# Optimization experiments

Measured on AMD Instinct MI355X. Metric: run time of the kernel, lower is better.

## Reference

```python
import jax, jax.numpy as jnp
import numpy as np
from jax import lax


def _conv1x1(x, w, b=None):
    # x: [N,C,H,W], w: [O,C]
    y = jnp.einsum('nchw,oc->nohw', x, w)
    if b is not None:
        y = y + b[None, :, None, None]
    return y


def _bn(x, g, b, rm, rv):
    # eval-mode BatchNorm2d, eps=1e-5 (torch default)
    inv = g / jnp.sqrt(rv + 1e-5)
    return x * inv[None, :, None, None] + (b - rm * inv)[None, :, None, None]


def setup_inputs() -> dict:
    key = jax.random.key(0)
    ks = jax.random.split(key, 32)
    N, C1, C2, H, W = 16, 256, 256, 64, 64
    mid = C2 // 16  # local_att reduction=16
    f32 = jnp.float32
    def nrm(k, shp, s=0.05):
        return s * jax.random.normal(k, shp, f32)
    return dict(
        x1=jax.random.normal(ks[0], (N, C1, H, W), f32),
        x2=jax.random.normal(ks[1], (N, C2, H, W), f32),
        conv1_w=nrm(ks[2], (C2, C1)), conv1_b=nrm(ks[3], (C2,)),
        conv2_w=nrm(ks[4], (C2, C2)), conv2_b=nrm(ks[5], (C2,)),
        conv3_w=nrm(ks[6], (C2, C2)), conv3_b=nrm(ks[7], (C2,)),
        conv4_w=nrm(ks[8], (C2, C2)), conv4_b=nrm(ks[9], (C2,)),
        conv4g_w=nrm(ks[10], (1, C2)), conv4g_b=nrm(ks[11], (1,)),
        bn_g=1.0 + nrm(ks[12], (C2,)), bn_b=nrm(ks[13], (C2,)),
        bn_rm=nrm(ks[14], (C2,)), bn_rv=1.0 + 0.1 * jax.random.uniform(ks[15], (C2,), f32),
        gamma=jax.random.normal(ks[16], (C2, 1, 1), f32), beta=jnp.zeros((C2, 1, 1), f32),
        gate_w=nrm(ks[17], (C2, C2)), gate_b=nrm(ks[18], (C2,)),
        dw_w=nrm(ks[19], (C2, 1, 3, 3)), dw_b=nrm(ks[20], (C2,)),
        interact_w=nrm(ks[21], (C2 // 4, C2 // 4)), interact_b=0.5 + nrm(ks[22], (C2 // 4,)),
        ca_w=nrm(ks[23], (1, 1, 5)),  # channel_att conv1d kernel, k=5 for C=256
        la1_w=nrm(ks[24], (mid, C2)),
        la_bn_g=1.0 + nrm(ks[25], (mid,)), la_bn_b=nrm(ks[26], (mid,)),
        la_bn_rm=nrm(ks[27], (mid,)), la_bn_rv=1.0 + 0.1 * jax.random.uniform(ks[28], (mid,), f32),
        fh_w=nrm(ks[29], (C2, mid)), fw_w=nrm(ks[30], (C2, mid)),
    )


def reference(x1, x2, conv1_w, conv1_b, conv2_w, conv2_b, conv3_w, conv3_b,
              conv4_w, conv4_b, conv4g_w, conv4g_b, bn_g, bn_b, bn_rm, bn_rv,
              gamma, beta, gate_w, gate_b, dw_w, dw_b, interact_w, interact_b,
              ca_w, la1_w, la_bn_g, la_bn_b, la_bn_rm, la_bn_rv, fh_w, fw_w):
    N, _, H, W = x1.shape
    C = conv1_w.shape[0]
    g1 = _conv1x1(x1, conv1_w, conv1_b)
    w1 = jax.nn.sigmoid(_bn(g1, bn_g, bn_b, bn_rm, bn_rv))
    g2 = _conv1x1(x2, conv2_w, conv2_b)
    w2 = jax.nn.sigmoid(_bn(g2, bn_g, bn_b, bn_rm, bn_rv))
    XG = g1 + g2

    # channel_att: GAP -> conv1d(k=5) across channels -> sigmoid gate
    y = XG.mean((2, 3))[:, None, :]  # [N,1,C]
    y = lax.conv_general_dilated(y, ca_w, (1,), [(2, 2)],
                                 dimension_numbers=('NCH', 'OIH', 'NCH'))
    temp = XG * jax.nn.sigmoid(y[:, 0, :])[:, :, None, None]

    # spatial sigmoid gate then 4-way group interact + softmax reweight
    Xs = jax.nn.sigmoid(_conv1x1(XG, conv4g_w, conv4g_b)) * XG
    C4 = C // 4
    Xr = Xs.reshape(N, 4, C4, H, W)
    o1 = jnp.einsum('ngchw,oc->ngohw', Xr, interact_w) + interact_b[None, None, :, None, None]
    xmap = o1.reshape(N, 4, 1, C4 * H * W)
    xav = xmap / xmap.mean(-1, keepdims=True)
    soft = jax.nn.softmax(xav, axis=2)  # softmax over size-1 dim -> ones (faithful)
    out = (soft.reshape(N, 4, C4, H, W) * Xr).reshape(N, C, H, W)

    # per-group (16) normalization using X_GOBAL stats (std unbiased, ddof=1)
    GN = 16
    xs = XG.reshape(N, GN, -1)
    mu = xs.mean(-1, keepdims=True)
    sd = jnp.std(xs, axis=-1, keepdims=True, ddof=1)
    x_gui = ((out.reshape(N, GN, -1) - mu) / (sd + 1e-10)).reshape(N, C, H, W)
    x_gui = x_gui * gamma[None] + beta[None]

    # threshold masks vs global-avg sigmoid reweights
    rw = jax.nn.sigmoid(XG.mean((2, 3), keepdims=True))  # [N,C,1,1]
    up1 = rw >= w1
    up2 = rw >= w2
    zero = jnp.zeros((), XG.dtype)
    x_up = jnp.where(up1, XG, zero) + jnp.where(up2, XG, zero)
    x_low = jnp.where(~up1, XG, zero) + jnp.where(~up2, XG, zero)

    # low branch: dwconv3x3 -> 1x1 -> channel-softmax gate
    dw = lax.conv_general_dilated(x_low, dw_w, (1, 1), [(1, 1), (1, 1)],
                                  dimension_numbers=('NCHW', 'OIHW', 'NCHW'),
                                  feature_group_count=C) + dw_b[None, :, None, None]
    x11 = _conv1x1(dw, conv3_w, conv3_b)
    gate = jax.nn.softmax(jax.nn.relu(x_low.mean((2, 3)) @ gate_w.T + gate_b), axis=1)
    xL = x11 * gate[:, :, None, None] + _conv1x1(x_up, conv4_w, conv4_b) + x_gui + temp

    # local_att (coordinate attention)
    xh = jnp.swapaxes(xL.mean(3, keepdims=True), 2, 3)  # [N,C,1,H]
    xw = xL.mean(2, keepdims=True)                       # [N,C,1,W]
    yc = jax.nn.relu(_bn(_conv1x1(jnp.concatenate([xh, xw], 3), la1_w),
                         la_bn_g, la_bn_b, la_bn_rm, la_bn_rv))
    sh = jax.nn.sigmoid(_conv1x1(jnp.swapaxes(yc[..., :H], 2, 3), fh_w))  # [N,C,H,1]
    sw = jax.nn.sigmoid(_conv1x1(yc[..., H:], fw_w))                      # [N,C,1,W]
    return xL * sh * sw
```

## Files before the change

kernel.cpp:

```cpp
#include <hip/hip_runtime.h>
#include <cstddef>
#include <cstdint>

constexpr int NN = 16, CC = 256, HH = 64, WW = 64, HW = 64 * 64;
constexpr size_t FSZ = (size_t)NN * CC * HW;

typedef short bf16x8 __attribute__((ext_vector_type(8)));
typedef float f32x4 __attribute__((ext_vector_type(4)));

__device__ __forceinline__ float sigmoidf_(float x) { return 1.f / (1.f + expf(-x)); }

__device__ __forceinline__ unsigned short bf16_rne(float f) {
    uint32_t u = __builtin_bit_cast(uint32_t, f);
    u += 0x7FFFu + ((u >> 16) & 1u);
    return (unsigned short)(u >> 16);
}
__device__ __forceinline__ float bf16_tof(unsigned short h) {
    uint32_t u = ((uint32_t)h) << 16;
    return __builtin_bit_cast(float, u);
}


__global__ __launch_bounds__(256) void wsplit_kernel(
    const float* __restrict__ w1, const float* __restrict__ w2,
    const float* __restrict__ w3, const float* __restrict__ w4,
    unsigned short* __restrict__ w1h, unsigned short* __restrict__ w1m, unsigned short* __restrict__ w1l,
    unsigned short* __restrict__ w2h, unsigned short* __restrict__ w2m, unsigned short* __restrict__ w2l,
    unsigned short* __restrict__ w4h, unsigned short* __restrict__ w4l,
    unsigned short* __restrict__ w3b,
    float* __restrict__ zstat, float* __restrict__ zspix) {
    const int i = blockIdx.x * 256 + threadIdx.x;
    const int o = i >> 8, c = i & 255;
    const size_t fo = ((size_t)((o >> 4) * 8 + (c >> 5))) * 512 +
                      (size_t)(((c & 31) >> 3) * 128 + (o & 15) * 8 + (c & 7));
    {
        float x = w1[i];
        unsigned short h = bf16_rne(x); float r = x - bf16_tof(h);
        unsigned short m = bf16_rne(r); float r2 = r - bf16_tof(m);
        w1h[fo] = h; w1m[fo] = m; w1l[fo] = bf16_rne(r2);
    }
    {
        float x = w2[i];
        unsigned short h = bf16_rne(x); float r = x - bf16_tof(h);
        unsigned short m = bf16_rne(r); float r2 = r - bf16_tof(m);
        w2h[fo] = h; w2m[fo] = m; w2l[fo] = bf16_rne(r2);
    }
    {
        float x = w4[i];
        unsigned short h = bf16_rne(x); float r = x - bf16_tof(h);
        w4h[fo] = h; w4l[fo] = bf16_rne(r);
    }
    w3b[fo] = bf16_rne(w3[i]);
    if (i < 8192) zstat[i] = 0.f;
    zspix[i] = 0.f;
}

template <int NS>
__global__ __launch_bounds__(256) void tsplit_kernel(const float* __restrict__ X,
                                                     unsigned short* __restrict__ O0,
                                                     unsigned short* __restrict__ O1,
                                                     unsigned short* __restrict__ O2) {
    const int hw0 = blockIdx.x * 64, c0 = blockIdx.y * 64, n = blockIdx.z;
    __shared__ float sT[64][65];
    const int tid = threadIdx.x;
    {
        const int hwl = (tid & 15) << 2;
        const int cl = tid >> 4;
#pragma unroll
        for (int p = 0; p < 4; ++p) {
            const int c = cl + p * 16;
            const float4 v = *(const float4*)(X + ((size_t)(n * CC + c0 + c)) * HW + hw0 + hwl);
            sT[c][hwl] = v.x; sT[c][hwl + 1] = v.y; sT[c][hwl + 2] = v.z; sT[c][hwl + 3] = v.w;
        }
    }
    __syncthreads();
    const int hwl = tid >> 2, cb = (tid & 3) << 4;
    unsigned short h[16], m[16], l[16];
#pragma unroll
    for (int j = 0; j < 16; ++j) {
        const float x = sT[cb + j][hwl];
        const unsigned short hh = bf16_rne(x);
        h[j] = hh;
        if (NS >= 2) {
            const float r = x - bf16_tof(hh);
            const unsigned short mm = bf16_rne(r);
            m[j] = mm;
            if (NS >= 3) l[j] = bf16_rne(r - bf16_tof(mm));
        }
    }
    const size_t ob = ((size_t)(n * HW + hw0 + hwl)) * 256 + c0 + cb;
    *(int4*)(O0 + ob) = *(int4*)&h[0]; *(int4*)(O0 + ob + 8) = *(int4*)&h[8];
    if (NS >= 2) { *(int4*)(O1 + ob) = *(int4*)&m[0]; *(int4*)(O1 + ob + 8) = *(int4*)&m[8]; }
    if (NS >= 3) { *(int4*)(O2 + ob) = *(int4*)&l[0]; *(int4*)(O2 + ob + 8) = *(int4*)&l[8]; }
}

template <int NS>
__device__ __forceinline__ void mfma_core5(const unsigned short* __restrict__ X0,
                                           const unsigned short* __restrict__ X1,
                                           const unsigned short* __restrict__ X2,
                                           const unsigned short* __restrict__ W0,
                                           const unsigned short* __restrict__ W1,
                                           const unsigned short* __restrict__ W2,
                                           int n, int hw0, int o0, f32x4 (&acc)[2][4]) {
    __shared__ unsigned short sX[2][NS][64][40];
    const int tid = threadIdx.x;
    const int lane = tid & 63, wv = tid >> 6, quad = lane >> 4, nlo = lane & 15;
    const int srow = tid >> 2, skoff = (tid & 3) << 3;
    const unsigned short* Xs[3] = {X0, X1, X2};
    const unsigned short* Ws[3] = {W0, W1, W2};
    const size_t xg = ((size_t)(n * HW + hw0 + srow)) * 256 + skoff;
    const unsigned short* wp[NS];
#pragma unroll
    for (int s = 0; s < NS; ++s)
        wp[s] = Ws[s] + ((size_t)((o0 >> 4) + wv) * 8) * 512 + (size_t)lane * 8;

    bf16x8 af[2][NS][2];
#pragma unroll
    for (int s = 0; s < NS; ++s)
        *(int4*)&sX[0][s][srow][skoff] = *(const int4*)(Xs[s] + xg);
#pragma unroll
    for (int s = 0; s < NS; ++s)
#pragma unroll
        for (int f = 0; f < 2; ++f)
            af[0][s][f] = *(const bf16x8*)(wp[s] + ((size_t)(f * 32)) * 512);
    __syncthreads();

#pragma unroll
    for (int ks = 0; ks < 8; ++ks) {
        const int cur = ks & 1;
        int4 nx[NS];
        if (ks < 7) {
#pragma unroll
            for (int s = 0; s < NS; ++s) nx[s] = *(const int4*)(Xs[s] + xg + (ks + 1) * 32);
#pragma unroll
            for (int s = 0; s < NS; ++s)
#pragma unroll
                for (int f = 0; f < 2; ++f)
                    af[cur ^ 1][s][f] = *(const bf16x8*)(wp[s] + ((size_t)(f * 32 + ks + 1)) * 512);
        }
#pragma unroll
        for (int nt = 0; nt < 4; ++nt) {
            bf16x8 bfr[NS];
#pragma unroll
            for (int s = 0; s < NS; ++s) bfr[s] = *(const bf16x8*)&sX[cur][s][nt * 16 + nlo][quad * 8];
#pragma unroll
            for (int f = 0; f < 2; ++f) {
                if (NS == 3) {
                    acc[f][nt] = __builtin_amdgcn_mfma_f32_16x16x32_bf16(af[cur][1][f], bfr[1], acc[f][nt], 0, 0, 0);
                    acc[f][nt] = __builtin_amdgcn_mfma_f32_16x16x32_bf16(af[cur][0][f], bfr[2], acc[f][nt], 0, 0, 0);
                    acc[f][nt] = __builtin_amdgcn_mfma_f32_16x16x32_bf16(af[cur][2][f], bfr[0], acc[f][nt], 0, 0, 0);
                    acc[f][nt] = __builtin_amdgcn_mfma_f32_16x16x32_bf16(af[cur][0][f], bfr[1], acc[f][nt], 0, 0, 0);
                    acc[f][nt] = __builtin_amdgcn_mfma_f32_16x16x32_bf16(af[cur][1][f], bfr[0], acc[f][nt], 0, 0, 0);
                    acc[f][nt] = __builtin_amdgcn_mfma_f32_16x16x32_bf16(af[cur][0][f], bfr[0], acc[f][nt], 0, 0, 0);
                } else if (NS == 2) {
                    acc[f][nt] = __builtin_amdgcn_mfma_f32_16x16x32_bf16(af[cur][0][f], bfr[1], acc[f][nt], 0, 0, 0);
                    acc[f][nt] = __builtin_amdgcn_mfma_f32_16x16x32_bf16(af[cur][1][f], bfr[0], acc[f][nt], 0, 0, 0);
                    acc[f][nt] = __builtin_amdgcn_mfma_f32_16x16x32_bf16(af[cur][0][f], bfr[0], acc[f][nt], 0, 0, 0);
                } else {
                    acc[f][nt] = __builtin_amdgcn_mfma_f32_16x16x32_bf16(af[cur][0][f], bfr[0], acc[f][nt], 0, 0, 0);
                }
            }
        }
        if (ks < 7) {
#pragma unroll
            for (int s = 0; s < NS; ++s) *(int4*)&sX[cur ^ 1][s][srow][skoff] = nx[s];
        }
        __syncthreads();
    }
}

__device__ __forceinline__ void mfma_core_pair(const unsigned short* __restrict__ XUH,
                                               const unsigned short* __restrict__ XUL,
                                               const unsigned short* __restrict__ XDW,
                                               const unsigned short* __restrict__ W4H,
                                               const unsigned short* __restrict__ W4L,
                                               const unsigned short* __restrict__ W3B,
                                               int n, int hw0, int o0,
                                               f32x4 (&acc_a)[2][4], f32x4 (&acc_b)[2][4]) {
    __shared__ unsigned short sX[2][3][64][40];
    const int tid = threadIdx.x;
    const int lane = tid & 63, wv = tid >> 6, quad = lane >> 4, nlo = lane & 15;
    const int srow = tid >> 2, skoff = (tid & 3) << 3;
    const unsigned short* Xs[3] = {XUH, XUL, XDW};
    const unsigned short* Ws[3] = {W4H, W4L, W3B};
    const size_t xg = ((size_t)(n * HW + hw0 + srow)) * 256 + skoff;
    const unsigned short* wp[3];
#pragma unroll
    for (int s = 0; s < 3; ++s)
        wp[s] = Ws[s] + ((size_t)((o0 >> 4) + wv) * 8) * 512 + (size_t)lane * 8;

    bf16x8 af[2][3][2];
#pragma unroll
    for (int s = 0; s < 3; ++s)
        *(int4*)&sX[0][s][srow][skoff] = *(const int4*)(Xs[s] + xg);
#pragma unroll
    for (int s = 0; s < 3; ++s)
#pragma unroll
        for (int f = 0; f < 2; ++f)
            af[0][s][f] = *(const bf16x8*)(wp[s] + ((size_t)(f * 32)) * 512);
    __syncthreads();

#pragma unroll
    for (int ks = 0; ks < 8; ++ks) {
        const int cur = ks & 1;
        int4 nx[3];
        if (ks < 7) {
#pragma unroll
            for (int s = 0; s < 3; ++s) nx[s] = *(const int4*)(Xs[s] + xg + (ks + 1) * 32);
#pragma unroll
            for (int s = 0; s < 3; ++s)
#pragma unroll
                for (int f = 0; f < 2; ++f)
                    af[cur ^ 1][s][f] = *(const bf16x8*)(wp[s] + ((size_t)(f * 32 + ks + 1)) * 512);
        }
#pragma unroll
        for (int nt = 0; nt < 4; ++nt) {
            bf16x8 bfr[3];
#pragma unroll
            for (int s = 0; s < 3; ++s) bfr[s] = *(const bf16x8*)&sX[cur][s][nt * 16 + nlo][quad * 8];
#pragma unroll
            for (int f = 0; f < 2; ++f) {
                acc_a[f][nt] = __builtin_amdgcn_mfma_f32_16x16x32_bf16(af[cur][0][f], bfr[1], acc_a[f][nt], 0, 0, 0);
                acc_a[f][nt] = __builtin_amdgcn_mfma_f32_16x16x32_bf16(af[cur][1][f], bfr[0], acc_a[f][nt], 0, 0, 0);
                acc_a[f][nt] = __builtin_amdgcn_mfma_f32_16x16x32_bf16(af[cur][0][f], bfr[0], acc_a[f][nt], 0, 0, 0);
                acc_b[f][nt] = __builtin_amdgcn_mfma_f32_16x16x32_bf16(af[cur][2][f], bfr[2], acc_b[f][nt], 0, 0, 0);
            }
        }
        if (ks < 7) {
#pragma unroll
            for (int s = 0; s < 3; ++s) *(int4*)&sX[cur ^ 1][s][srow][skoff] = nx[s];
        }
        __syncthreads();
    }
}

template <int NS>
__global__ __launch_bounds__(256, 3) void gemm_mfma_kernel(
    const unsigned short* __restrict__ X0, const unsigned short* __restrict__ X1,
    const unsigned short* __restrict__ X2, const unsigned short* __restrict__ W0,
    const unsigned short* __restrict__ W1, const unsigned short* __restrict__ W2,
    const float* __restrict__ bias, float* __restrict__ Y) {
    const int hw0 = blockIdx.x * 64, o0 = blockIdx.y * 128, n = blockIdx.z;
    f32x4 acc[2][4] = {};
    mfma_core5<NS>(X0, X1, X2, W0, W1, W2, n, hw0, o0, acc);
    const int lane = threadIdx.x & 63, wv = threadIdx.x >> 6;
    const int quad = lane >> 4, nlo = lane & 15;
#pragma unroll
    for (int f = 0; f < 2; ++f) {
        const int om = o0 + f * 64 + wv * 16 + quad * 4;
#pragma unroll
        for (int nt = 0; nt < 4; ++nt) {
            const int hw = hw0 + nt * 16 + nlo;
#pragma unroll
            for (int r = 0; r < 4; ++r) {
                const int o = om + r;
                Y[((size_t)(n * CC + o)) * HW + hw] = acc[f][nt][r] + bias[o];
            }
        }
    }
}

__global__ __launch_bounds__(256, 3) void gemm_xg_kernel(
    const unsigned short* __restrict__ X0, const unsigned short* __restrict__ X1,
    const unsigned short* __restrict__ X2, const unsigned short* __restrict__ W0,
    const unsigned short* __restrict__ W1, const unsigned short* __restrict__ W2,
    const float* __restrict__ bias, const float* __restrict__ g1,
    const float* __restrict__ cgw,
    float* __restrict__ XG, float* __restrict__ sum_c, float* __restrict__ sq_c,
    float* __restrict__ s_pix) {
    const int hw0 = blockIdx.x * 64, o0 = blockIdx.y * 128, n = blockIdx.z;
    f32x4 acc[2][4] = {};
    mfma_core5<3>(X0, X1, X2, W0, W1, W2, n, hw0, o0, acc);
    __shared__ float sRed[4][64];
    const int lane = threadIdx.x & 63, wv = threadIdx.x >> 6;
    const int quad = lane >> 4, nlo = lane & 15;
    float pnt[4] = {0.f, 0.f, 0.f, 0.f};
#pragma unroll
    for (int f = 0; f < 2; ++f) {
        const int om = o0 + f * 64 + wv * 16 + quad * 4;
#pragma unroll
        for (int r = 0; r < 4; ++r) {
            const int o = om + r;
            const float b = bias[o];
            const float wg = cgw[o];
            float s = 0.f, q = 0.f;
#pragma unroll
            for (int nt = 0; nt < 4; ++nt) {
                const int hw = hw0 + nt * 16 + nlo;
                const size_t rowi = ((size_t)(n * CC + o)) * HW + hw;
                const float xgv = acc[f][nt][r] + b + g1[rowi];
                XG[rowi] = xgv;
                s += xgv; q += xgv * xgv;
                pnt[nt] += wg * xgv;
            }
#pragma unroll
            for (int off = 1; off < 16; off <<= 1) { s += __shfl_xor(s, off); q += __shfl_xor(q, off); }
            if (nlo == 0) { atomicAdd(&sum_c[n * CC + o], s); atomicAdd(&sq_c[n * CC + o], q); }
        }
    }
#pragma unroll
    for (int nt = 0; nt < 4; ++nt) {
        float p = pnt[nt];
        p += __shfl_xor(p, 16); p += __shfl_xor(p, 32);
        if (quad == 0) sRed[wv][nt * 16 + nlo] = p;
    }
    __syncthreads();
    if (threadIdx.x < 64) {
        const float s2 = sRed[0][threadIdx.x] + sRed[1][threadIdx.x] +
                         sRed[2][threadIdx.x] + sRed[3][threadIdx.x];
        atomicAdd(&s_pix[n * HW + hw0 + threadIdx.x], s2);
    }
}

__global__ __launch_bounds__(256, 3) void gemm_final_kernel(
    const unsigned short* __restrict__ XUH, const unsigned short* __restrict__ XUL,
    const unsigned short* __restrict__ XDW,
    const unsigned short* __restrict__ W4H, const unsigned short* __restrict__ W4L,
    const unsigned short* __restrict__ W3B,
    const float* __restrict__ b3, const float* __restrict__ b4,
    const float* __restrict__ XG, const float* __restrict__ s_pix,
    const float* __restrict__ cgb,
    const float* __restrict__ gate, const float* __restrict__ ca_sig,
    const float* __restrict__ mu_g, const float* __restrict__ isd_g,
    const float* __restrict__ gamma, const float* __restrict__ beta,
    float* __restrict__ out) {
    const int hw0 = blockIdx.x * 64, o0 = blockIdx.y * 128, n = blockIdx.z;
    f32x4 acc_a[2][4] = {};
    f32x4 acc_b[2][4] = {};
    mfma_core_pair(XUH, XUL, XDW, W4H, W4L, W3B, n, hw0, o0, acc_a, acc_b);
    const int lane = threadIdx.x & 63, wv = threadIdx.x >> 6;
    const int quad = lane >> 4, nlo = lane & 15;
    const float cgb0 = cgb[0];
#pragma unroll
    for (int f = 0; f < 2; ++f) {
        const int om = o0 + f * 64 + wv * 16 + quad * 4;
#pragma unroll
        for (int nt = 0; nt < 4; ++nt) {
            const int hw = hw0 + nt * 16 + nlo;
            const int pix = n * HW + hw;
            const float sp = sigmoidf_(s_pix[pix] + cgb0);
#pragma unroll
            for (int r = 0; r < 4; ++r) {
                const int o = om + r;
                const float g = gate[n * CC + o];
                const float cs = ca_sig[n * CC + o];
                const float mu = mu_g[n * 16 + (o >> 4)];
                const float isd = isd_g[n * 16 + (o >> 4)];
                const size_t rowi = ((size_t)(n * CC + o)) * HW + hw;
                const float xg = XG[rowi];
                const float gui = (sp * xg - mu) * isd * gamma[o] + beta[o];
                out[rowi] = (acc_b[f][nt][r] + b3[o]) * g + (acc_a[f][nt][r] + b4[o]) + gui + xg * cs;
            }
        }
    }
}

__global__ __launch_bounds__(256) void stats2_kernel(const float* __restrict__ sum_c,
                                                     const float* __restrict__ sq_c,
                                                     const float* __restrict__ caw,
                                                     float* __restrict__ rw,
                                                     float* __restrict__ ca_sig,
                                                     float* __restrict__ mu_g,
                                                     float* __restrict__ isd_g,
                                                     float* __restrict__ xlow_sum) {
    const int n = blockIdx.x, c = threadIdx.x;
    __shared__ float m[256];
    const float mean = sum_c[n * CC + c] * (1.f / (float)HW);
    m[c] = mean;
    rw[n * CC + c] = sigmoidf_(mean);
    xlow_sum[n * CC + c] = 0.f;
    __syncthreads();
    float y = 0.f;
#pragma unroll
    for (int k = 0; k < 5; ++k) {
        const int cc = c - 2 + k;
        if (cc >= 0 && cc < 256) y += m[cc] * caw[k];
    }
    ca_sig[n * CC + c] = sigmoidf_(y);
    if (c < 16) {
        float S = 0.f, Q = 0.f;
        for (int j = 0; j < 16; ++j) {
            S += sum_c[n * CC + c * 16 + j];
            Q += sq_c[n * CC + c * 16 + j];
        }
        const float cnt = 65536.f;
        const float mu = S / cnt;
        float var = (Q - S * S / cnt) * (1.f / (cnt - 1.f));
        var = fmaxf(var, 0.f);
        mu_g[n * 16 + c] = mu;
        isd_g[n * 16 + c] = 1.f / (sqrtf(var) + 1e-10f);
    }
}

__global__ __launch_bounds__(256) void masks_split_kernel(
    float* g1_xlow,
    const float* __restrict__ XG,
    const float* __restrict__ rw,
    const float* __restrict__ bng, const float* __restrict__ bnb,
    const float* __restrict__ bnrm, const float* __restrict__ bnrv,
    unsigned short* __restrict__ O0, unsigned short* __restrict__ O1,
    float* __restrict__ xlow_sum) {
    const int hw0 = blockIdx.x * 64, c0 = blockIdx.y * 64, n = blockIdx.z;
    __shared__ float sT[64][65];
    const int tid = threadIdx.x;
    const int cl = tid >> 2;
    const int q = tid & 3;
    const int c = c0 + cl;
    const float inv = bng[c] / sqrtf(bnrv[c] + 1e-5f);
    const float off = bnb[c] - bnrm[c] * inv;
    const float rwv = rw[n * CC + c];
    const size_t rowb = ((size_t)(n * CC + c)) * HW + hw0;
    float lsum = 0.f;
#pragma unroll
    for (int j = 0; j < 4; ++j) {
        const int hwl = q * 4 + j * 16;
        const float4 a = *(const float4*)(g1_xlow + rowb + hwl);
        const float4 x = *(const float4*)(XG + rowb + hwl);
        const float* ap = &a.x; const float* xp = &x.x;
        float4 xlv;
        float* xlp = &xlv.x;
#pragma unroll
        for (int e = 0; e < 4; ++e) {
            const float g2e = xp[e] - ap[e];
            const float w1 = sigmoidf_(inv * ap[e] + off);
            const float w2 = sigmoidf_(inv * g2e + off);
            const float cu = (rwv >= w1 ? 1.f : 0.f) + (rwv >= w2 ? 1.f : 0.f);
            const float xu = xp[e] * cu;
            const float xl = xp[e] * (2.f - cu);
            sT[cl][hwl + e] = xu;
            xlp[e] = xl;
            lsum += xl;
        }
        *(float4*)(g1_xlow + rowb + hwl) = xlv;
    }
    lsum += __shfl_xor(lsum, 1);
    lsum += __shfl_xor(lsum, 2);
    if (q == 0) atomicAdd(&xlow_sum[n * CC + c], lsum);
    __syncthreads();
    const int hwl2 = tid >> 2, cb = (tid & 3) << 4;
    unsigned short h[16], m[16];
#pragma unroll
    for (int j = 0; j < 16; ++j) {
        const float x = sT[cb + j][hwl2];
        const unsigned short hh = bf16_rne(x);
        h[j] = hh;
        m[j] = bf16_rne(x - bf16_tof(hh));
    }
    const size_t ob = ((size_t)(n * HW + hw0 + hwl2)) * 256 + c0 + cb;
    *(int4*)(O0 + ob) = *(int4*)&h[0]; *(int4*)(O0 + ob + 8) = *(int4*)&h[8];
    *(int4*)(O1 + ob) = *(int4*)&m[0]; *(int4*)(O1 + ob + 8) = *(int4*)&m[8];
}

__global__ __launch_bounds__(256) void gate_kernel(const float* __restrict__ xlow_sum,
                                                   const float* __restrict__ gatew,
                                                   const float* __restrict__ gateb,
                                                   float* __restrict__ gate) {
    const int n = blockIdx.x, c = threadIdx.x;
    __shared__ float xm[256];
    __shared__ float red[256];
    xm[c] = xlow_sum[n * CC + c] * (1.f / (float)HW);
    __syncthreads();
    float acc = gateb[c];
    const float* wr = gatew + (size_t)c * 256;
#pragma unroll 8
    for (int k = 0; k < 256; ++k) acc += xm[k] * wr[k];
    const float v = fmaxf(acc, 0.f);
    red[c] = v;
    __syncthreads();
    for (int s = 128; s > 0; s >>= 1) {
        if (c < s) red[c] = fmaxf(red[c], red[c + s]);
        __syncthreads();
    }
    const float mx = red[0];
    __syncthreads();
    const float e = expf(v - mx);
    red[c] = e;
    __syncthreads();
    for (int s = 128; s > 0; s >>= 1) {
        if (c < s) red[c] += red[c + s];
        __syncthreads();
    }
    gate[n * CC + c] = e / red[0];
}

__global__ __launch_bounds__(256) void dwconv_kernel(const float* __restrict__ xlow,
                                                     const float* __restrict__ dww,
                                                     const float* __restrict__ dwb,
                                                     float* __restrict__ out) {
    const int c = blockIdx.x & 255;
    __shared__ float sl[64][65];
    const size_t base = (size_t)blockIdx.x * HW;
    for (int r = 0; r < 16; ++r) {
        const int idx = threadIdx.x + r * 256;
        sl[idx >> 6][idx & 63] = xlow[base + idx];
    }
    float wk[9];
#pragma unroll
    for (int j = 0; j < 9; ++j) wk[j] = dww[c * 9 + j];
    const float bias = dwb[c];
    __syncthreads();
    for (int r = 0; r < 16; ++r) {
        const int idx = threadIdx.x + r * 256;
        const int h = idx >> 6, w = idx & 63;
        float acc = bias;
#pragma unroll
        for (int dh = 0; dh < 3; ++dh) {
            const int hh = h + dh - 1;
            if (hh < 0 || hh > 63) continue;
#pragma unroll
            for (int dw2 = 0; dw2 < 3; ++dw2) {
                const int ww2 = w + dw2 - 1;
                if (ww2 < 0 || ww2 > 63) continue;
                acc += sl[hh][ww2] * wk[dh * 3 + dw2];
            }
        }
        out[base + idx] = acc;
    }
}

__global__ __launch_bounds__(256) void pool_kernel(const float* __restrict__ xL,
                                                   float* __restrict__ xh,
                                                   float* __restrict__ xw) {
    __shared__ float sl[64][65];
    const size_t base = (size_t)blockIdx.x * HW;
    for (int r = 0; r < 16; ++r) {
        const int idx = threadIdx.x + r * 256;
        sl[idx >> 6][idx & 63] = xL[base + idx];
    }
    __syncthreads();
    const int t = threadIdx.x;
    if (t < 64) {
        float s = 0.f;
        for (int w = 0; w < 64; ++w) s += sl[t][w];
        xh[(size_t)blockIdx.x * 64 + t] = s * (1.f / 64.f);
    } else if (t < 128) {
        const int w = t - 64;
        float s = 0.f;
        for (int h = 0; h < 64; ++h) s += sl[h][w];
        xw[(size_t)blockIdx.x * 64 + w] = s * (1.f / 64.f);
    }
}

__global__ __launch_bounds__(256) void local_att_kernel(const float* __restrict__ xh,
                                                        const float* __restrict__ xw,
                                                        const float* __restrict__ la1w,
                                                        const float* __restrict__ lag,
                                                        const float* __restrict__ lab,
                                                        const float* __restrict__ larm,
                                                        const float* __restrict__ larv,
                                                        const float* __restrict__ fhw,
                                                        const float* __restrict__ fww,
                                                        float* __restrict__ sh,
                                                        float* __restrict__ sw) {
    const int n = blockIdx.x;
    __shared__ float w1s[16 * 256];
    __shared__ float fhs[256 * 16];
    __shared__ float fws[256 * 16];
    __shared__ float ycs[16][128];
    for (int i = threadIdx.x; i < 4096; i += 256) {
        w1s[i] = la1w[i];
        fhs[i] = fhw[i];
        fws[i] = fww[i];
    }
    __syncthreads();
    for (int idx = threadIdx.x; idx < 2048; idx += 256) {
        const int m = idx >> 7, p = idx & 127;
        const float* vsrc = (p < 64) ? (xh + (size_t)n * CC * 64 + p)
                                     : (xw + (size_t)n * CC * 64 + (p - 64));
        float acc = 0.f;
#pragma unroll 8
        for (int c = 0; c < 256; ++c) acc += w1s[m * 256 + c] * vsrc[(size_t)c * 64];
        const float inv = lag[m] / sqrtf(larv[m] + 1e-5f);
        const float off = lab[m] - larm[m] * inv;
        ycs[m][p] = fmaxf(inv * acc + off, 0.f);
    }
    __syncthreads();
    for (int idx = threadIdx.x; idx < 16384; idx += 256) {
        const int c = idx >> 6, h = idx & 63;
        float a1 = 0.f, a2 = 0.f;
#pragma unroll
        for (int m = 0; m < 16; ++m) {
            a1 += fhs[c * 16 + m] * ycs[m][h];
            a2 += fws[c * 16 + m] * ycs[m][64 + h];
        }
        sh[(size_t)n * CC * 64 + idx] = sigmoidf_(a1);
        sw[(size_t)n * CC * 64 + idx] = sigmoidf_(a2);
    }
}

__global__ __launch_bounds__(256) void final_kernel(const float* __restrict__ xL,
                                                    const float* __restrict__ sh,
                                                    const float* __restrict__ sw,
                                                    float* __restrict__ out) {
    __shared__ float shs[64], sws[64];
    const int t = threadIdx.x;
    if (t < 64) shs[t] = sh[(size_t)blockIdx.x * 64 + t];
    else if (t < 128) sws[t - 64] = sw[(size_t)blockIdx.x * 64 + (t - 64)];
    __syncthreads();
    const size_t base = (size_t)blockIdx.x * HW;
#pragma unroll 4
    for (int r = 0; r < 16; ++r) {
        const int idx = t + r * 256;
        out[base + idx] = xL[base + idx] * shs[idx >> 6] * sws[idx & 63];
    }
}

extern "C" void kernel_launch(void* const* d_in, const int* in_sizes, int n_in,
                              void* d_out, int out_size, void* d_ws, size_t ws_size,
                              hipStream_t stream) {
    const float* x1 = (const float*)d_in[0];
    const float* x2 = (const float*)d_in[1];
    const float* c1w = (const float*)d_in[2];
    const float* c1b = (const float*)d_in[3];
    const float* c2w = (const float*)d_in[4];
    const float* c2b = (const float*)d_in[5];
    const float* c3w = (const float*)d_in[6];
    const float* c3b = (const float*)d_in[7];
    const float* c4w = (const float*)d_in[8];
    const float* c4b = (const float*)d_in[9];
    const float* cgw = (const float*)d_in[10];
    const float* cgb = (const float*)d_in[11];
    const float* bng = (const float*)d_in[12];
    const float* bnb = (const float*)d_in[13];
    const float* bnrm = (const float*)d_in[14];
    const float* bnrv = (const float*)d_in[15];
    const float* gamma = (const float*)d_in[16];
    const float* beta = (const float*)d_in[17];
    const float* gatew = (const float*)d_in[18];
    const float* gateb = (const float*)d_in[19];
    const float* dww = (const float*)d_in[20];
    const float* dwb = (const float*)d_in[21];
    const float* caw = (const float*)d_in[24];
    const float* la1w = (const float*)d_in[25];
    const float* lag = (const float*)d_in[26];
    const float* lab = (const float*)d_in[27];
    const float* larm = (const float*)d_in[28];
    const float* larv = (const float*)d_in[29];
    const float* fhw = (const float*)d_in[30];
    const float* fww = (const float*)d_in[31];

    float* ws = (float*)d_ws;
    float* buf0 = ws;
    float* buf1 = ws + FSZ;
    float* buf2 = ws + 2 * FSZ;
    float* sp = ws + 3 * FSZ;
    float* sum_c = sp;    sp += 4096;
    float* sq_c = sp;     sp += 4096;
    float* rw = sp;       sp += 4096;
    float* ca_sig = sp;   sp += 4096;
    float* xlow_sum = sp; sp += 4096;
    float* mu_g = sp;     sp += 256;
    float* isd_g = sp;    sp += 256;
    float* s_pix = sp;    sp += (size_t)NN * HW;
    float* xh = sp;       sp += (size_t)NN * CC * 64;
    float* xwb = sp;      sp += (size_t)NN * CC * 64;
    float* shb = sp;      sp += (size_t)NN * CC * 64;
    float* swb = sp;      sp += (size_t)NN * CC * 64;
    unsigned short* wsp = (unsigned short*)shb;
    unsigned short* w1h = wsp + 0 * 65536;
    unsigned short* w1m = wsp + 1 * 65536;
    unsigned short* w1l = wsp + 2 * 65536;
    unsigned short* w2h = wsp + 3 * 65536;
    unsigned short* w2m = wsp + 4 * 65536;
    unsigned short* w2l = wsp + 5 * 65536;
    unsigned short* w4h = wsp + 6 * 65536;
    unsigned short* w4l = wsp + 7 * 65536;
    unsigned short* w3b = wsp + 8 * 65536;

    float* out = (float*)d_out;

    const dim3 gt(HW / 64, CC / 64, NN);
    const dim3 gg(HW / 64, CC / 128, NN);

    wsplit_kernel<<<256, 256, 0, stream>>>(c1w, c2w, c3w, c4w, w1h, w1m, w1l,
                                           w2h, w2m, w2l, w4h, w4l, w3b,
                                           sum_c, s_pix);
    {
        unsigned short* sx0 = (unsigned short*)buf1;
        unsigned short* sx1 = (unsigned short*)buf1 + FSZ;
        unsigned short* sx2 = (unsigned short*)buf2;
        tsplit_kernel<3><<<gt, 256, 0, stream>>>(x1, sx0, sx1, sx2);
        gemm_mfma_kernel<3><<<gg, 256, 0, stream>>>(sx0, sx1, sx2, w1h, w1m, w1l, c1b, buf0);
    }
    {
        unsigned short* sx0 = (unsigned short*)out;
        unsigned short* sx1 = (unsigned short*)out + FSZ;
        unsigned short* sx2 = (unsigned short*)buf2;
        tsplit_kernel<3><<<gt, 256, 0, stream>>>(x2, sx0, sx1, sx2);
        gemm_xg_kernel<<<gg, 256, 0, stream>>>(sx0, sx1, sx2, w2h, w2m, w2l, c2b,
                                               buf0, cgw, buf1, sum_c, sq_c, s_pix);
    }
    stats2_kernel<<<NN, 256, 0, stream>>>(sum_c, sq_c, caw, rw, ca_sig, mu_g, isd_g, xlow_sum);
    {
        unsigned short* ux0 = (unsigned short*)out;
        unsigned short* ux1 = (unsigned short*)out + FSZ;
        masks_split_kernel<<<gt, 256, 0, stream>>>(buf0, buf1, rw, bng, bnb, bnrm, bnrv,
                                                   ux0, ux1, xlow_sum);
    }
    float* gate = sum_c;
    gate_kernel<<<NN, 256, 0, stream>>>(xlow_sum, gatew, gateb, gate);
    dwconv_kernel<<<NN * CC, 256, 0, stream>>>(buf0, dww, dwb, buf0);
    {
        unsigned short* sx0 = (unsigned short*)buf2;
        tsplit_kernel<1><<<gt, 256, 0, stream>>>(buf0, sx0, nullptr, nullptr);
    }
    {
        unsigned short* ux0 = (unsigned short*)out;
        unsigned short* ux1 = (unsigned short*)out + FSZ;
        unsigned short* sx0 = (unsigned short*)buf2;
        gemm_final_kernel<<<gg, 256, 0, stream>>>(ux0, ux1, sx0, w4h, w4l, w3b,
                                                  c3b, c4b, buf1, s_pix, cgb,
                                                  gate, ca_sig, mu_g, isd_g, gamma, beta,
                                                  buf0);
    }
    pool_kernel<<<NN * CC, 256, 0, stream>>>(buf0, xh, xwb);
    local_att_kernel<<<NN, 256, 0, stream>>>(xh, xwb, la1w, lag, lab, larm, larv,
                                             fhw, fww, shb, swb);
    final_kernel<<<NN * CC, 256, 0, stream>>>(buf0, shb, swb, out);
}
```

Measured before the change: 654.0 us.

## Stream GEMM activation tiles directly to LDS with XOR-swizzled layout

The MFMA GEMM cores now use global_load_lds (direct global-to-LDS 16-byte loads) instead of loading into registers and then storing to shared memory. The LDS tile drops its padded row stride of 40 in favour of 32 with an XOR swizzle on the 8-element chunk index, so fragment reads avoid bank conflicts without padding. This is meant to cut VGPR pressure and the extra LDS write instructions, and to shrink LDS use. The risk is that the async LDS loads are ordered only by the existing __syncthreads (no explicit vmcnt wait), so correctness depends on the barrier draining them.

```diff
diff --git a/kernel.cpp b/kernel.cpp
--- a/kernel.cpp
+++ b/kernel.cpp
@@ -18,6 +18,11 @@
 __device__ __forceinline__ float bf16_tof(unsigned short h) {
     uint32_t u = ((uint32_t)h) << 16;
     return __builtin_bit_cast(float, u);
+}
+
+__device__ __forceinline__ void gload16(const void* g, void* l) {
+    __builtin_amdgcn_global_load_lds((const __attribute__((address_space(1))) void*)g,
+                                     (__attribute__((address_space(3))) void*)l, 16, 0, 0);
 }
 
 
@@ -95,29 +100,37 @@
 }
 
 template <int NS>
-__device__ __forceinline__ void mfma_core5(const unsigned short* __restrict__ X0,
+__device__ __forceinline__ void mfma_core6(const unsigned short* __restrict__ X0,
                                            const unsigned short* __restrict__ X1,
                                            const unsigned short* __restrict__ X2,
                                            const unsigned short* __restrict__ W0,
                                            const unsigned short* __restrict__ W1,
                                            const unsigned short* __restrict__ W2,
                                            int n, int hw0, int o0, f32x4 (&acc)[2][4]) {
-    __shared__ unsigned short sX[2][NS][64][40];
+    __shared__ unsigned short sX[2][NS][64][32];
     const int tid = threadIdx.x;
     const int lane = tid & 63, wv = tid >> 6, quad = lane >> 4, nlo = lane & 15;
-    const int srow = tid >> 2, skoff = (tid & 3) << 3;
+    const int srow = tid >> 2;
+    const int schunk = (tid & 3) ^ ((srow >> 1) & 3);
     const unsigned short* Xs[3] = {X0, X1, X2};
     const unsigned short* Ws[3] = {W0, W1, W2};
-    const size_t xg = ((size_t)(n * HW + hw0 + srow)) * 256 + skoff;
+    const size_t xg = ((size_t)(n * HW + hw0 + srow)) * 256 + schunk * 8;
     const unsigned short* wp[NS];
 #pragma unroll
     for (int s = 0; s < NS; ++s)
         wp[s] = Ws[s] + ((size_t)((o0 >> 4) + wv) * 8) * 512 + (size_t)lane * 8;
 
+    int roff[4];
+#pragma unroll
+    for (int nt = 0; nt < 4; ++nt) {
+        const int rrow = nt * 16 + nlo;
+        roff[nt] = rrow * 32 + (quad ^ ((rrow >> 1) & 3)) * 8;
+    }
+
     bf16x8 af[2][NS][2];
 #pragma unroll
     for (int s = 0; s < NS; ++s)
-        *(int4*)&sX[0][s][srow][skoff] = *(const int4*)(Xs[s] + xg);
+        gload16(Xs[s] + xg, &sX[0][s][wv * 16][0]);
 #pragma unroll
     for (int s = 0; s < NS; ++s)
 #pragma unroll
@@ -128,10 +141,10 @@
 #pragma unroll
     for (int ks = 0; ks < 8; ++ks) {
         const int cur = ks & 1;
-        int4 nx[NS];
         if (ks < 7) {
 #pragma unroll
-            for (int s = 0; s < NS; ++s) nx[s] = *(const int4*)(Xs[s] + xg + (ks + 1) * 32);
+            for (int s = 0; s < NS; ++s)
+                gload16(Xs[s] + xg + (ks + 1) * 32, &sX[cur ^ 1][s][wv * 16][0]);
 #pragma unroll
             for (int s = 0; s < NS; ++s)
 #pragma unroll
@@ -142,7 +155,8 @@
         for (int nt = 0; nt < 4; ++nt) {
             bf16x8 bfr[NS];
 #pragma unroll
-            for (int s = 0; s < NS; ++s) bfr[s] = *(const bf16x8*)&sX[cur][s][nt * 16 + nlo][quad * 8];
+            for (int s = 0; s < NS; ++s)
+                bfr[s] = *(const bf16x8*)&sX[cur][s][0][roff[nt]];
 #pragma unroll
             for (int f = 0; f < 2; ++f) {
                 if (NS == 3) {
@@ -161,10 +175,6 @@
                 }
             }
         }
-        if (ks < 7) {
-#pragma unroll
-            for (int s = 0; s < NS; ++s) *(int4*)&sX[cur ^ 1][s][srow][skoff] = nx[s];
-        }
         __syncthreads();
     }
 }
@@ -177,22 +187,30 @@
                                                const unsigned short* __restrict__ W3B,
                                                int n, int hw0, int o0,
                                                f32x4 (&acc_a)[2][4], f32x4 (&acc_b)[2][4]) {
-    __shared__ unsigned short sX[2][3][64][40];
+    __shared__ unsigned short sX[2][3][64][32];
     const int tid = threadIdx.x;
     const int lane = tid & 63, wv = tid >> 6, quad = lane >> 4, nlo = lane & 15;
-    const int srow = tid >> 2, skoff = (tid & 3) << 3;
+    const int srow = tid >> 2;
+    const int schunk = (tid & 3) ^ ((srow >> 1) & 3);
     const unsigned short* Xs[3] = {XUH, XUL, XDW};
     const unsigned short* Ws[3] = {W4H, W4L, W3B};
-    const size_t xg = ((size_t)(n * HW + hw0 + srow)) * 256 + skoff;
+    const size_t xg = ((size_t)(n * HW + hw0 + srow)) * 256 + schunk * 8;
     const unsigned short* wp[3];
 #pragma unroll
     for (int s = 0; s < 3; ++s)
         wp[s] = Ws[s] + ((size_t)((o0 >> 4) + wv) * 8) * 512 + (size_t)lane * 8;
 
+    int roff[4];
+#pragma unroll
+    for (int nt = 0; nt < 4; ++nt) {
+        const int rrow = nt * 16 + nlo;
+        roff[nt] = rrow * 32 + (quad ^ ((rrow >> 1) & 3)) * 8;
+    }
+
     bf16x8 af[2][3][2];
 #pragma unroll
     for (int s = 0; s < 3; ++s)
-        *(int4*)&sX[0][s][srow][skoff] = *(const int4*)(Xs[s] + xg);
+        gload16(Xs[s] + xg, &sX[0][s][wv * 16][0]);
 #pragma unroll
     for (int s = 0; s < 3; ++s)
 #pragma unroll
@@ -203,10 +221,10 @@
 #pragma unroll
     for (int ks = 0; ks < 8; ++ks) {
         const int cur = ks & 1;
-        int4 nx[3];
         if (ks < 7) {
 #pragma unroll
-            for (int s = 0; s < 3; ++s) nx[s] = *(const int4*)(Xs[s] + xg + (ks + 1) * 32);
+            for (int s = 0; s < 3; ++s)
+                gload16(Xs[s] + xg + (ks + 1) * 32, &sX[cur ^ 1][s][wv * 16][0]);
 #pragma unroll
             for (int s = 0; s < 3; ++s)
 #pragma unroll
@@ -217,7 +235,8 @@
         for (int nt = 0; nt < 4; ++nt) {
             bf16x8 bfr[3];
 #pragma unroll
-            for (int s = 0; s < 3; ++s) bfr[s] = *(const bf16x8*)&sX[cur][s][nt * 16 + nlo][quad * 8];
+            for (int s = 0; s < 3; ++s)
+                bfr[s] = *(const bf16x8*)&sX[cur][s][0][roff[nt]];
 #pragma unroll
             for (int f = 0; f < 2; ++f) {
                 acc_a[f][nt] = __builtin_amdgcn_mfma_f32_16x16x32_bf16(af[cur][0][f], bfr[1], acc_a[f][nt], 0, 0, 0);
@@ -225,10 +244,6 @@
                 acc_a[f][nt] = __builtin_amdgcn_mfma_f32_16x16x32_bf16(af[cur][0][f], bfr[0], acc_a[f][nt], 0, 0, 0);
                 acc_b[f][nt] = __builtin_amdgcn_mfma_f32_16x16x32_bf16(af[cur][2][f], bfr[2], acc_b[f][nt], 0, 0, 0);
             }
-        }
-        if (ks < 7) {
-#pragma unroll
-            for (int s = 0; s < 3; ++s) *(int4*)&sX[cur ^ 1][s][srow][skoff] = nx[s];
         }
         __syncthreads();
     }
@@ -242,7 +257,7 @@
     const float* __restrict__ bias, float* __restrict__ Y) {
     const int hw0 = blockIdx.x * 64, o0 = blockIdx.y * 128, n = blockIdx.z;
     f32x4 acc[2][4] = {};
-    mfma_core5<NS>(X0, X1, X2, W0, W1, W2, n, hw0, o0, acc);
+    mfma_core6<NS>(X0, X1, X2, W0, W1, W2, n, hw0, o0, acc);
     const int lane = threadIdx.x & 63, wv = threadIdx.x >> 6;
     const int quad = lane >> 4, nlo = lane & 15;
 #pragma unroll
@@ -270,7 +285,7 @@
     float* __restrict__ s_pix) {
     const int hw0 = blockIdx.x * 64, o0 = blockIdx.y * 128, n = blockIdx.z;
     f32x4 acc[2][4] = {};
-    mfma_core5<3>(X0, X1, X2, W0, W1, W2, n, hw0, o0, acc);
+    mfma_core6<3>(X0, X1, X2, W0, W1, W2, n, hw0, o0, acc);
     __shared__ float sRed[4][64];
     const int lane = threadIdx.x & 63, wv = threadIdx.x >> 6;
     const int quad = lane >> 4, nlo = lane & 15;
```

Measured after the change: 645.4 us. Within noise of the previous version (-1.3%).
